# Kernel tuning notes

Hardware: AMD Instinct MI355X
Metric: run time of the kernel (lower is better)

The kernel has to match this reference:

```python
import jax, jax.numpy as jnp
import numpy as np

N = 16384          # tokens (batch*seq)
D = 2048           # input_dim
H = 2 * D          # router hidden dim
E = 64             # num_experts
NUM_SHARED = 8
TOP_K = 2


def setup_inputs() -> dict:
    key = jax.random.key(0)
    k_x, k_w1, k_b1, k_w2, k_b2 = jax.random.split(key, 5)
    s1 = 1.0 / np.sqrt(D)
    s2 = 1.0 / np.sqrt(H)
    return {
        "x": jax.random.normal(k_x, (N, D), dtype=jnp.float32),
        "W1": jax.random.uniform(k_w1, (D, H), jnp.float32, -s1, s1),
        "b1": jax.random.uniform(k_b1, (H,), jnp.float32, -s1, s1),
        "W2": jax.random.uniform(k_w2, (H, E), jnp.float32, -s2, s2),
        "b2": jax.random.uniform(k_b2, (E,), jnp.float32, -s2, s2),
    }


def reference(x, W1, b1, W2, b2):
    # router MLP: linear -> exact (erf) GELU -> linear -> softmax
    h = jax.nn.gelu(x @ W1 + b1, approximate=False)          # [N, H]
    weights = jax.nn.softmax(h @ W2 + b2, axis=-1)            # [N, E]
    global_weights = weights[:, :NUM_SHARED]                  # [N, num_shared]
    local = weights[:, NUM_SHARED:]                           # [N, E - num_shared]
    local_weights, local_indices = jax.lax.top_k(local, TOP_K)  # [N, top_k] each
    return (global_weights, local_weights, local_indices, weights)
```

## Files before the change

kernel.cpp:

```cpp
#include <hip/hip_runtime.h>
#include <math.h>

namespace {
constexpr int kN = 16384;
constexpr int kD = 2048;
constexpr int kH = 4096;
constexpr int kE = 64;
constexpr int kShared = 8;

constexpr int OFF_GW = 0;
constexpr int OFF_LW = kN * kShared;
constexpr int OFF_LI = OFF_LW + kN * 2;
constexpr int OFF_W  = OFF_LI + kN * 2;

constexpr int GS_STRIDE = 132;
constexpr int HSPLIT = 4;
constexpr int CHUNKS = 8;

constexpr size_t XH_OFF  = 0;
constexpr size_t XL_OFF  = (size_t)kN * kD;
constexpr size_t W1TH_OFF = XL_OFF + (size_t)kN * kD;
constexpr size_t W1TL_OFF = W1TH_OFF + (size_t)kH * kD;
constexpr size_t WS_BASE = (W1TL_OFF + (size_t)kH * kD) * 2;
constexpr size_t PART_FLOAT_OFF = WS_BASE / 4;
constexpr size_t WS_FULL = WS_BASE + (size_t)HSPLIT * kN * kE * 4;

constexpr int BUF_FLOATS = 64 * GS_STRIDE;
constexpr int BUF_F16    = BUF_FLOATS * 2;
}

typedef _Float16 half8  __attribute__((ext_vector_type(8)));
typedef _Float16 half4t __attribute__((ext_vector_type(4)));
typedef float    f32x16 __attribute__((ext_vector_type(16)));

__device__ __forceinline__ void async16(const _Float16* g, _Float16* l) {
    __builtin_amdgcn_global_load_lds(
        (const __attribute__((address_space(1))) void*)g,
        (__attribute__((address_space(3))) void*)l, 16, 0, 0);
}

__global__ __launch_bounds__(256)
void convert_x(const float* __restrict__ x, _Float16* __restrict__ xh,
               _Float16* __restrict__ xl)
{
    const size_t i = ((size_t)blockIdx.x * 256 + threadIdx.x) * 4;
    const float4 v = *reinterpret_cast<const float4*>(x + i);
    half4t h, l;
    const float vs[4] = {v.x, v.y, v.z, v.w};
    #pragma unroll
    for (int j = 0; j < 4; ++j) {
        const _Float16 hj = (_Float16)vs[j];
        h[j] = hj;
        l[j] = (_Float16)((vs[j] - (float)hj) * 2048.0f);
    }
    *reinterpret_cast<half4t*>(xh + i) = h;
    *reinterpret_cast<half4t*>(xl + i) = l;
}

__global__ __launch_bounds__(256)
void convert_w1t(const float* __restrict__ W1, _Float16* __restrict__ th,
                 _Float16* __restrict__ tl)
{
    __shared__ float T[64][65];
    const int bk = blockIdx.x & 31;
    const int bn = blockIdx.x >> 5;
    const int k0 = bk * 64, n0 = bn * 64;
    const int t = threadIdx.x;
    const int c4 = (t & 15) * 4, r = t >> 4;

    #pragma unroll
    for (int i = 0; i < 4; ++i) {
        const int kk = r + 16 * i;
        const float4 v = *reinterpret_cast<const float4*>(
            W1 + (size_t)(k0 + kk) * kH + n0 + c4);
        T[kk][c4 + 0] = v.x; T[kk][c4 + 1] = v.y;
        T[kk][c4 + 2] = v.z; T[kk][c4 + 3] = v.w;
    }
    __syncthreads();
    #pragma unroll
    for (int i = 0; i < 4; ++i) {
        const int nn = r + 16 * i;
        half4t h, l;
        #pragma unroll
        for (int j = 0; j < 4; ++j) {
            const float vv = T[c4 + j][nn];
            const _Float16 hj = (_Float16)vv;
            h[j] = hj;
            l[j] = (_Float16)((vv - (float)hj) * 2048.0f);
        }
        *reinterpret_cast<half4t*>(th + (size_t)(n0 + nn) * kD + k0 + c4) = h;
        *reinterpret_cast<half4t*>(tl + (size_t)(n0 + nn) * kD + k0 + c4) = l;
    }
}

__global__ __launch_bounds__(256, 2)
void gemm1_mfma(const _Float16* __restrict__ xh, const float* __restrict__ b1,
                const float* __restrict__ W2, float* __restrict__ dst,
                int atomicMode)
{
    __shared__ __align__(16) float smem[2 * BUF_FLOATS];

    const int t = threadIdx.x;
    const int lane = t & 63;
    const int w = t >> 6;
    const int bx = blockIdx.x;
    const int hSplit = bx & 3;
    const int rowBlock = bx >> 2;
    const int rowBase = rowBlock * 128;

    const int mw = (w >> 1) * 64;
    const int nc32 = (w & 1) * 32;

    unsigned int gofsA[4], gofsB[4];
    #pragma unroll
    for (int i = 0; i < 8; ++i) {
        const int c = i * 256 + t;
        const int tile = c >> 9;
        const int s = c & 511;
        const int row = s >> 2;
        const int pq = s & 3;
        const int q = pq ^ (row & 3) ^ ((row >> 2) & 3);
        const unsigned int plane =
            (tile == 0) ? (unsigned int)XH_OFF :
            (tile == 1) ? (unsigned int)XL_OFF :
            (tile == 2) ? (unsigned int)W1TH_OFF : (unsigned int)W1TL_OFF;
        if (tile < 2)
            gofsA[i] = plane + (unsigned int)(rowBase + row) * kD + q * 8;
        else
            gofsB[i - 4] = plane + (unsigned int)row * kD + q * 8;
    }

    int aOff[2][2], bOff[2][2];
    #pragma unroll
    for (int mt = 0; mt < 2; ++mt)
        #pragma unroll
        for (int ks = 0; ks < 2; ++ks) {
            const int row = mw + mt * 32 + (lane & 31);
            const int q = (lane >> 5) + 2 * ks;
            aOff[mt][ks] = row * 32 + ((q ^ (row & 3) ^ ((row >> 2) & 3)) * 8);
        }
    #pragma unroll
    for (int nt = 0; nt < 2; ++nt)
        #pragma unroll
        for (int ks = 0; ks < 2; ++ks) {
            const int row = nt * 64 + nc32 + (lane & 31);
            const int q = (lane >> 5) + 2 * ks;
            bOff[nt][ks] = row * 32 + ((q ^ (row & 3) ^ ((row >> 2) & 3)) * 8);
        }

    const int g_r0 = (t >> 3) * 4;
    const int g_e0 = (t & 7) * 8;
    float lacc[4][8];
    #pragma unroll
    for (int i = 0; i < 4; ++i)
        #pragma unroll
        for (int j = 0; j < 8; ++j) lacc[i][j] = 0.0f;

    auto stageA = [&](int buf, int nk) {
        _Float16* l = (_Float16*)smem + (size_t)buf * BUF_F16;
        #pragma unroll
        for (int i = 0; i < 4; ++i)
            async16(xh + gofsA[i] + nk, l + ((i * 256 + t) * 8));
    };
    auto stageB = [&](int buf, int nc, int nk) {
        _Float16* l = (_Float16*)smem + (size_t)buf * BUF_F16;
        const unsigned int hOff =
            (unsigned int)(hSplit * (CHUNKS * 128) + nc * 128) * kD;
        #pragma unroll
        for (int i = 0; i < 4; ++i)
            async16(xh + gofsB[i] + hOff + nk, l + (((i + 4) * 256 + t) * 8));
    };

    int cur = 0;
    stageA(0, 0);
    stageB(0, 0, 0);

    for (int chunk = 0; chunk < CHUNKS; ++chunk) {
        const int hBase = hSplit * (CHUNKS * 128) + chunk * 128;

        f32x16 accH[2][2], accL[2][2];
        #pragma unroll
        for (int a = 0; a < 2; ++a)
            #pragma unroll
            for (int b = 0; b < 2; ++b)
                #pragma unroll
                for (int r = 0; r < 16; ++r) { accH[a][b][r] = 0.0f; accL[a][b][r] = 0.0f; }

        for (int kt = 0; kt < kD; kt += 32) {
            const bool isLast = (chunk == CHUNKS - 1) && (kt == kD - 32);
            int nc = chunk, nk = kt + 32;
            if (nk == kD) { nc = chunk + 1; nk = 0; }

            const _Float16* lds = (const _Float16*)smem + (size_t)cur * BUF_F16;
            const int nbuf = cur ^ 1;

            if (!isLast) {
                stageA(nbuf, nk);
                asm volatile("s_waitcnt vmcnt(4)" ::: "memory");
            } else {
                asm volatile("s_waitcnt vmcnt(0)" ::: "memory");
            }
            __builtin_amdgcn_s_barrier();
            asm volatile("" ::: "memory");

            {
                half8 aH[2], aL[2], bH[2], bL[2];
                #pragma unroll
                for (int mt = 0; mt < 2; ++mt) {
                    aH[mt] = *reinterpret_cast<const half8*>(lds + aOff[mt][0]);
                    aL[mt] = *reinterpret_cast<const half8*>(lds + 4096 + aOff[mt][0]);
                }
                #pragma unroll
                for (int nt = 0; nt < 2; ++nt) {
                    bH[nt] = *reinterpret_cast<const half8*>(lds + 8192 + bOff[nt][0]);
                    bL[nt] = *reinterpret_cast<const half8*>(lds + 12288 + bOff[nt][0]);
                }
                __builtin_amdgcn_s_setprio(1);
                #pragma unroll
                for (int mt = 0; mt < 2; ++mt)
                    #pragma unroll
                    for (int nt = 0; nt < 2; ++nt) {
                        accH[mt][nt] = __builtin_amdgcn_mfma_f32_32x32x16_f16(
                            aH[mt], bH[nt], accH[mt][nt], 0, 0, 0);
                        accL[mt][nt] = __builtin_amdgcn_mfma_f32_32x32x16_f16(
                            aH[mt], bL[nt], accL[mt][nt], 0, 0, 0);
                        accL[mt][nt] = __builtin_amdgcn_mfma_f32_32x32x16_f16(
                            aL[mt], bH[nt], accL[mt][nt], 0, 0, 0);
                    }
                __builtin_amdgcn_s_setprio(0);
                __builtin_amdgcn_sched_barrier(0);
            }
            asm volatile("" ::: "memory");
            __builtin_amdgcn_s_barrier();
            asm volatile("" ::: "memory");

            {
                half8 aH[2], aL[2], bH[2], bL[2];
                #pragma unroll
                for (int mt = 0; mt < 2; ++mt) {
                    aH[mt] = *reinterpret_cast<const half8*>(lds + aOff[mt][1]);
                    aL[mt] = *reinterpret_cast<const half8*>(lds + 4096 + aOff[mt][1]);
                }
                #pragma unroll
                for (int nt = 0; nt < 2; ++nt) {
                    bH[nt] = *reinterpret_cast<const half8*>(lds + 8192 + bOff[nt][1]);
                    bL[nt] = *reinterpret_cast<const half8*>(lds + 12288 + bOff[nt][1]);
                }
                if (!isLast) stageB(nbuf, nc, nk);
                __builtin_amdgcn_s_setprio(1);
                #pragma unroll
                for (int mt = 0; mt < 2; ++mt)
                    #pragma unroll
                    for (int nt = 0; nt < 2; ++nt) {
                        accH[mt][nt] = __builtin_amdgcn_mfma_f32_32x32x16_f16(
                            aH[mt], bH[nt], accH[mt][nt], 0, 0, 0);
                        accL[mt][nt] = __builtin_amdgcn_mfma_f32_32x32x16_f16(
                            aH[mt], bL[nt], accL[mt][nt], 0, 0, 0);
                        accL[mt][nt] = __builtin_amdgcn_mfma_f32_32x32x16_f16(
                            aL[mt], bH[nt], accL[mt][nt], 0, 0, 0);
                    }
                __builtin_amdgcn_s_setprio(0);
                __builtin_amdgcn_sched_barrier(0);
            }
            asm volatile("s_waitcnt lgkmcnt(0)" ::: "memory");
            __builtin_amdgcn_s_barrier();
            asm volatile("" ::: "memory");
            cur ^= 1;
        }

        float* gS = smem + (size_t)(cur ^ 1) * BUF_FLOATS;
        const float inv2048 = 1.0f / 2048.0f;
        const int hl = nc32 + (lane & 31);
        for (int hf = 0; hf < 2; ++hf) {
            if (hf) {
                asm volatile("s_waitcnt lgkmcnt(0)" ::: "memory");
                __builtin_amdgcn_s_barrier();
                asm volatile("" ::: "memory");
            }
            const float bb = b1[hBase + hf * 64 + hl];
            #pragma unroll
            for (int mt = 0; mt < 2; ++mt) {
                #pragma unroll
                for (int rq = 0; rq < 4; ++rq) {
                    float vr[4];
                    #pragma unroll
                    for (int rr = 0; rr < 4; ++rr) {
                        const int r = rq * 4 + rr;
                        const float hv = accH[mt][hf][r] + accL[mt][hf][r] * inv2048 + bb;
                        vr[rr] = 0.5f * hv * (1.0f + erff(hv * 0.70710678118654752f));
                    }
                    const int mrow = mw + mt * 32 + 8 * rq + 4 * (lane >> 5);
                    *reinterpret_cast<float4*>(gS + hl * GS_STRIDE + mrow) =
                        make_float4(vr[0], vr[1], vr[2], vr[3]);
                }
            }
            asm volatile("s_waitcnt lgkmcnt(0)" ::: "memory");
            __builtin_amdgcn_s_barrier();
            asm volatile("" ::: "memory");
            const float* W2p = W2 + (size_t)(hBase + hf * 64) * kE + g_e0;
            #pragma unroll 4
            for (int h = 0; h < 64; ++h) {
                const float4 gv = *reinterpret_cast<const float4*>(gS + h * GS_STRIDE + g_r0);
                const float4 w0 = *reinterpret_cast<const float4*>(W2p + (size_t)h * kE);
                const float4 w1 = *reinterpret_cast<const float4*>(W2p + (size_t)h * kE + 4);
                const float ga[4] = {gv.x, gv.y, gv.z, gv.w};
                const float wb[8] = {w0.x, w0.y, w0.z, w0.w, w1.x, w1.y, w1.z, w1.w};
                #pragma unroll
                for (int i = 0; i < 4; ++i)
                    #pragma unroll
                    for (int j = 0; j < 8; ++j)
                        lacc[i][j] = fmaf(ga[i], wb[j], lacc[i][j]);
            }
        }
        asm volatile("s_waitcnt lgkmcnt(0)" ::: "memory");
        __builtin_amdgcn_s_barrier();
        asm volatile("" ::: "memory");
    }

    if (atomicMode) {
        #pragma unroll
        for (int i = 0; i < 4; ++i)
            #pragma unroll
            for (int j = 0; j < 8; ++j)
                atomicAdd(dst + (size_t)(rowBase + g_r0 + i) * kE + g_e0 + j, lacc[i][j]);
    } else {
        float* drow = dst + ((size_t)hSplit * kN + rowBase + g_r0) * kE + g_e0;
        #pragma unroll
        for (int i = 0; i < 4; ++i) {
            *reinterpret_cast<float4*>(drow + (size_t)i * kE) =
                make_float4(lacc[i][0], lacc[i][1], lacc[i][2], lacc[i][3]);
            *reinterpret_cast<float4*>(drow + (size_t)i * kE + 4) =
                make_float4(lacc[i][4], lacc[i][5], lacc[i][6], lacc[i][7]);
        }
    }
}

__global__ __launch_bounds__(256, 2)
void gemm1_kernel(const float* __restrict__ x, const float* __restrict__ W1,
                  const float* __restrict__ b1, const float* __restrict__ W2,
                  float* __restrict__ logits)
{
    __shared__ __align__(16) float smem[64 * GS_STRIDE];
    float* As = smem;
    float* Bs = smem + 32 * 128;
    float* gS = smem;

    const int t  = threadIdx.x;
    const int bx = blockIdx.x;
    const int rowBlock = bx >> 2;
    const int hSplit   = bx & 3;
    const int rowBase  = rowBlock * 128;
    const int hBase0   = hSplit * 1024;

    const int ty = t >> 4;
    const int tx = t & 15;
    const int r0 = ty * 8;
    const int c0 = tx * 8;
    const int g_r0 = (t >> 3) * 4;
    const int g_e0 = (t & 7) * 8;

    float lacc[4][8];
    #pragma unroll
    for (int i = 0; i < 4; ++i)
        #pragma unroll
        for (int j = 0; j < 8; ++j) lacc[i][j] = 0.0f;

    for (int chunk = 0; chunk < 8; ++chunk) {
        const int hBase = hBase0 + chunk * 128;
        float C[8][8];
        #pragma unroll
        for (int i = 0; i < 8; ++i)
            #pragma unroll
            for (int j = 0; j < 8; ++j) C[i][j] = 0.0f;

        for (int kt = 0; kt < kD; kt += 32) {
            __syncthreads();
            #pragma unroll
            for (int i = 0; i < 4; ++i) {
                const int f  = t + 256 * i;
                const int m  = f >> 3;
                const int kq = (f & 7) * 4;
                const float4 v = *reinterpret_cast<const float4*>(
                    x + (size_t)(rowBase + m) * kD + kt + kq);
                As[(kq + 0) * 128 + m] = v.x;
                As[(kq + 1) * 128 + m] = v.y;
                As[(kq + 2) * 128 + m] = v.z;
                As[(kq + 3) * 128 + m] = v.w;
            }
            #pragma unroll
            for (int i = 0; i < 4; ++i) {
                const int f  = t + 256 * i;
                const int k  = f >> 5;
                const int n4 = (f & 31) * 4;
                *reinterpret_cast<float4*>(Bs + k * 128 + n4) =
                    *reinterpret_cast<const float4*>(W1 + (size_t)(kt + k) * kH + hBase + n4);
            }
            __syncthreads();
            #pragma unroll 8
            for (int k = 0; k < 32; ++k) {
                const float4 a0 = *reinterpret_cast<const float4*>(As + k * 128 + r0);
                const float4 a1 = *reinterpret_cast<const float4*>(As + k * 128 + r0 + 4);
                const float4 b0 = *reinterpret_cast<const float4*>(Bs + k * 128 + c0);
                const float4 b1v = *reinterpret_cast<const float4*>(Bs + k * 128 + c0 + 4);
                const float a[8] = {a0.x, a0.y, a0.z, a0.w, a1.x, a1.y, a1.z, a1.w};
                const float b[8] = {b0.x, b0.y, b0.z, b0.w, b1v.x, b1v.y, b1v.z, b1v.w};
                #pragma unroll
                for (int i = 0; i < 8; ++i)
                    #pragma unroll
                    for (int j = 0; j < 8; ++j)
                        C[i][j] = fmaf(a[i], b[j], C[i][j]);
            }
        }

        #pragma unroll
        for (int j = 0; j < 8; ++j) {
            const float bb = b1[hBase + c0 + j];
            #pragma unroll
            for (int i = 0; i < 8; ++i) {
                const float hv = C[i][j] + bb;
                C[i][j] = 0.5f * hv * (1.0f + erff(hv * 0.70710678118654752f));
            }
        }

        for (int half = 0; half < 2; ++half) {
            __syncthreads();
            if ((tx >> 3) == half) {
                const int hloc0 = c0 - half * 64;
                #pragma unroll
                for (int j = 0; j < 8; ++j) {
                    const float4 col = make_float4(C[0][j], C[1][j], C[2][j], C[3][j]);
                    const float4 col2 = make_float4(C[4][j], C[5][j], C[6][j], C[7][j]);
                    *reinterpret_cast<float4*>(gS + (hloc0 + j) * GS_STRIDE + r0)     = col;
                    *reinterpret_cast<float4*>(gS + (hloc0 + j) * GS_STRIDE + r0 + 4) = col2;
                }
            }
            __syncthreads();
            const float* W2p = W2 + (size_t)(hBase + half * 64) * kE + g_e0;
            #pragma unroll 4
            for (int h = 0; h < 64; ++h) {
                const float4 gv = *reinterpret_cast<const float4*>(gS + h * GS_STRIDE + g_r0);
                const float4 w0 = *reinterpret_cast<const float4*>(W2p + (size_t)h * kE);
                const float4 w1 = *reinterpret_cast<const float4*>(W2p + (size_t)h * kE + 4);
                const float ga[4] = {gv.x, gv.y, gv.z, gv.w};
                const float wb[8] = {w0.x, w0.y, w0.z, w0.w, w1.x, w1.y, w1.z, w1.w};
                #pragma unroll
                for (int i = 0; i < 4; ++i)
                    #pragma unroll
                    for (int j = 0; j < 8; ++j)
                        lacc[i][j] = fmaf(ga[i], wb[j], lacc[i][j]);
            }
        }
    }

    #pragma unroll
    for (int i = 0; i < 4; ++i)
        #pragma unroll
        for (int j = 0; j < 8; ++j)
            atomicAdd(logits + (size_t)(rowBase + g_r0 + i) * kE + g_e0 + j, lacc[i][j]);
}

__global__ __launch_bounds__(256)
void router_kernel(const float* __restrict__ b2, const float* __restrict__ src,
                   int atomicMode, float* __restrict__ out)
{
    const int lane = threadIdx.x & 63;
    const int row  = blockIdx.x * 4 + (threadIdx.x >> 6);

    float logit;
    if (atomicMode) {
        logit = src[(size_t)row * kE + lane] + b2[lane];
    } else {
        const float* p = src + (size_t)row * kE + lane;
        logit = p[0] + p[(size_t)kN * kE] + p[(size_t)2 * kN * kE] +
                p[(size_t)3 * kN * kE] + b2[lane];
    }

    float m = logit;
    #pragma unroll
    for (int off = 32; off > 0; off >>= 1) m = fmaxf(m, __shfl_xor(m, off));
    const float p = expf(logit - m);
    float s = p;
    #pragma unroll
    for (int off = 32; off > 0; off >>= 1) s += __shfl_xor(s, off);
    const float w = p / s;

    out[OFF_W + (size_t)row * kE + lane] = w;
    if (lane < kShared) out[OFF_GW + (size_t)row * kShared + lane] = w;

    float v1 = (lane >= kShared) ? w : -1.0f;
    int   i1 = lane - kShared;
    #pragma unroll
    for (int off = 32; off > 0; off >>= 1) {
        const float ov = __shfl_xor(v1, off);
        const int   oi = __shfl_xor(i1, off);
        if (ov > v1 || (ov == v1 && oi < i1)) { v1 = ov; i1 = oi; }
    }
    float v2 = (lane >= kShared && (lane - kShared) != i1) ? w : -1.0f;
    int   i2 = lane - kShared;
    #pragma unroll
    for (int off = 32; off > 0; off >>= 1) {
        const float ov = __shfl_xor(v2, off);
        const int   oi = __shfl_xor(i2, off);
        if (ov > v2 || (ov == v2 && oi < i2)) { v2 = ov; i2 = oi; }
    }
    if (lane == 0) {
        out[OFF_LW + (size_t)row * 2 + 0] = v1;
        out[OFF_LW + (size_t)row * 2 + 1] = v2;
        out[OFF_LI + (size_t)row * 2 + 0] = (float)i1;
        out[OFF_LI + (size_t)row * 2 + 1] = (float)i2;
    }
}

extern "C" void kernel_launch(void* const* d_in, const int* in_sizes, int n_in,
                              void* d_out, int out_size, void* d_ws, size_t ws_size,
                              hipStream_t stream)
{
    const float* x  = (const float*)d_in[0];
    const float* W1 = (const float*)d_in[1];
    const float* b1 = (const float*)d_in[2];
    const float* W2 = (const float*)d_in[3];
    const float* b2 = (const float*)d_in[4];
    float* out = (float*)d_out;
    float* logits = out + OFF_W;

    if (ws_size >= WS_BASE) {
        _Float16* base = (_Float16*)d_ws;
        const int atomicMode = (ws_size >= WS_FULL) ? 0 : 1;
        float* dst = atomicMode ? logits : ((float*)d_ws + PART_FLOAT_OFF);
        if (atomicMode)
            hipMemsetAsync(logits, 0, (size_t)kN * kE * sizeof(float), stream);
        hipLaunchKernelGGL(convert_x, dim3(kN * kD / 1024), dim3(256), 0, stream,
                           x, base + XH_OFF, base + XL_OFF);
        hipLaunchKernelGGL(convert_w1t, dim3((kD / 64) * (kH / 64)), dim3(256), 0, stream,
                           W1, base + W1TH_OFF, base + W1TL_OFF);
        hipLaunchKernelGGL(gemm1_mfma, dim3((kN / 128) * HSPLIT), dim3(256), 0, stream,
                           base + XH_OFF, b1, W2, dst, atomicMode);
        hipLaunchKernelGGL(router_kernel, dim3(kN / 4), dim3(256), 0, stream,
                           b2, dst, atomicMode, out);
    } else {
        hipMemsetAsync(logits, 0, (size_t)kN * kE * sizeof(float), stream);
        hipLaunchKernelGGL(gemm1_kernel, dim3((kN / 128) * 4), dim3(256), 0, stream,
                           x, W1, b1, W2, logits);
        hipLaunchKernelGGL(router_kernel, dim3(kN / 4), dim3(256), 0, stream,
                           b2, logits, 1, out);
    }
}
```

Before: 1.247 ms.

## Fuse x/W1 conversion kernels, remap GEMM blocks per XCD, move B staging earlier

Merges the x split-fp16 conversion and the W1 transpose-conversion into one launch, with each x block now handling four chunks. Remaps gemm1 block indices so that blocks landing on the same XCD (bx&7) share row blocks and hSplit pairs, aiming for better L2 reuse of the A and W1 tiles. Moves the next-B-tile async staging from the second half-step to the first, giving the loads more time to overlap with MFMA work, at some risk of LDS buffer hazards if the double-buffer timing is off.

```diff
diff --git a/kernel.cpp b/kernel.cpp
--- a/kernel.cpp
+++ b/kernel.cpp
@@ -27,6 +27,8 @@
 
 constexpr int BUF_FLOATS = 64 * GS_STRIDE;
 constexpr int BUF_F16    = BUF_FLOATS * 2;
+
+constexpr int CXB = 8192;
 }
 
 typedef _Float16 half8  __attribute__((ext_vector_type(8)));
@@ -40,32 +42,38 @@
 }
 
 __global__ __launch_bounds__(256)
-void convert_x(const float* __restrict__ x, _Float16* __restrict__ xh,
-               _Float16* __restrict__ xl)
-{
-    const size_t i = ((size_t)blockIdx.x * 256 + threadIdx.x) * 4;
-    const float4 v = *reinterpret_cast<const float4*>(x + i);
-    half4t h, l;
-    const float vs[4] = {v.x, v.y, v.z, v.w};
-    #pragma unroll
-    for (int j = 0; j < 4; ++j) {
-        const _Float16 hj = (_Float16)vs[j];
-        h[j] = hj;
-        l[j] = (_Float16)((vs[j] - (float)hj) * 2048.0f);
-    }
-    *reinterpret_cast<half4t*>(xh + i) = h;
-    *reinterpret_cast<half4t*>(xl + i) = l;
-}
-
-__global__ __launch_bounds__(256)
-void convert_w1t(const float* __restrict__ W1, _Float16* __restrict__ th,
-                 _Float16* __restrict__ tl)
+void convert_xw(const float* __restrict__ x, _Float16* __restrict__ xh,
+                _Float16* __restrict__ xl,
+                const float* __restrict__ W1, _Float16* __restrict__ th,
+                _Float16* __restrict__ tl)
 {
     __shared__ float T[64][65];
-    const int bk = blockIdx.x & 31;
-    const int bn = blockIdx.x >> 5;
+    const int b = blockIdx.x;
+    const int t = threadIdx.x;
+
+    if (b < CXB) {
+        #pragma unroll
+        for (int it = 0; it < 4; ++it) {
+            const size_t i = (((size_t)it * CXB + b) * 256 + t) * 4;
+            const float4 v = *reinterpret_cast<const float4*>(x + i);
+            half4t h, l;
+            const float vs[4] = {v.x, v.y, v.z, v.w};
+            #pragma unroll
+            for (int j = 0; j < 4; ++j) {
+                const _Float16 hj = (_Float16)vs[j];
+                h[j] = hj;
+                l[j] = (_Float16)((vs[j] - (float)hj) * 2048.0f);
+            }
+            *reinterpret_cast<half4t*>(xh + i) = h;
+            *reinterpret_cast<half4t*>(xl + i) = l;
+        }
+        return;
+    }
+
+    const int bb = b - CXB;
+    const int bk = bb & 31;
+    const int bn = bb >> 5;
     const int k0 = bk * 64, n0 = bn * 64;
-    const int t = threadIdx.x;
     const int c4 = (t & 15) * 4, r = t >> 4;
 
     #pragma unroll
@@ -104,8 +112,10 @@
     const int lane = t & 63;
     const int w = t >> 6;
     const int bx = blockIdx.x;
-    const int hSplit = bx & 3;
-    const int rowBlock = bx >> 2;
+    const int xcd = bx & 7;
+    const int j8 = bx >> 3;
+    const int hSplit = 2 * (xcd & 1) + (j8 & 1);
+    const int rowBlock = (xcd >> 1) * 32 + (j8 >> 1);
     const int rowBase = rowBlock * 128;
 
     const int mw = (w >> 1) * 64;
@@ -215,6 +225,7 @@
                     bH[nt] = *reinterpret_cast<const half8*>(lds + 8192 + bOff[nt][0]);
                     bL[nt] = *reinterpret_cast<const half8*>(lds + 12288 + bOff[nt][0]);
                 }
+                if (!isLast) stageB(nbuf, nc, nk);
                 __builtin_amdgcn_s_setprio(1);
                 #pragma unroll
                 for (int mt = 0; mt < 2; ++mt)
@@ -246,7 +257,6 @@
                     bH[nt] = *reinterpret_cast<const half8*>(lds + 8192 + bOff[nt][1]);
                     bL[nt] = *reinterpret_cast<const half8*>(lds + 12288 + bOff[nt][1]);
                 }
-                if (!isLast) stageB(nbuf, nc, nk);
                 __builtin_amdgcn_s_setprio(1);
                 #pragma unroll
                 for (int mt = 0; mt < 2; ++mt)
@@ -529,9 +539,8 @@
         float* dst = atomicMode ? logits : ((float*)d_ws + PART_FLOAT_OFF);
         if (atomicMode)
             hipMemsetAsync(logits, 0, (size_t)kN * kE * sizeof(float), stream);
-        hipLaunchKernelGGL(convert_x, dim3(kN * kD / 1024), dim3(256), 0, stream,
-                           x, base + XH_OFF, base + XL_OFF);
-        hipLaunchKernelGGL(convert_w1t, dim3((kD / 64) * (kH / 64)), dim3(256), 0, stream,
+        hipLaunchKernelGGL(convert_xw, dim3(CXB + (kD / 64) * (kH / 64)), dim3(256), 0, stream,
+                           x, base + XH_OFF, base + XL_OFF,
                            W1, base + W1TH_OFF, base + W1TL_OFF);
         hipLaunchKernelGGL(gemm1_mfma, dim3((kN / 128) * HSPLIT), dim3(256), 0, stream,
                            base + XH_OFF, b1, W2, dst, atomicMode);
```

Result: no change. 1.225 ms (-1.7%).
